# Kernel tuning notes

Hardware: AMD Instinct MI355X
Metric: run time of the kernel (lower is better)

The kernel has to match this reference:

```python
import jax, jax.numpy as jnp
import numpy as np

N = 100000       # nodes
E = 3200000      # directed edges (before self-loops)
D_IN, D_H, D_OUT = 512, 128, 64


def setup_inputs() -> dict:
    key = jax.random.key(0)
    k = jax.random.split(key, 6)
    x = jax.random.normal(k[0], (N, D_IN), jnp.float32)
    edge_index = jax.random.randint(k[1], (2, E), 0, N, dtype=jnp.int32)
    # Glorot-style init, matching GCNConv's linear weights
    W1 = jax.random.normal(k[2], (D_IN, D_H), jnp.float32) * np.float32(1.0 / np.sqrt(D_IN))
    b1 = jnp.zeros((D_H,), jnp.float32)
    W2 = jax.random.normal(k[3], (D_H, D_OUT), jnp.float32) * np.float32(1.0 / np.sqrt(D_H))
    b2 = jnp.zeros((D_OUT,), jnp.float32)
    return {"x": x, "edge_index": edge_index, "W1": W1, "b1": b1, "W2": W2, "b2": b2}


def _gcn_layer(h, src, dst, norm, W, b):
    # GCNConv: transform, then normalized gather/scatter-add aggregation
    h = h @ W                                  # [N, F_out]
    msg = h[src] * norm[:, None]               # gather + per-edge scale
    agg = jax.ops.segment_sum(msg, dst, num_segments=N)  # scatter-add
    return agg + b


def reference(x, edge_index, W1, b1, W2, b2):
    # add self-loops (GCNConv default add_self_loops=True)
    loops = jnp.arange(N, dtype=edge_index.dtype)
    src = jnp.concatenate([edge_index[0], loops])
    dst = jnp.concatenate([edge_index[1], loops])
    # symmetric normalization: D^{-1/2} (A+I) D^{-1/2}
    deg = jax.ops.segment_sum(jnp.ones_like(dst, dtype=x.dtype), dst, num_segments=N)
    dinv = jax.lax.rsqrt(jnp.maximum(deg, 1.0))  # deg >= 1 because of self-loops
    norm = dinv[src] * dinv[dst]                 # per-edge weight
    h = jax.nn.relu(_gcn_layer(x, src, dst, norm, W1, b1))
    return _gcn_layer(h, src, dst, norm, W2, b2)
```

## Files before the change

### kernel.cpp

```cpp
#include <hip/hip_runtime.h>
#include <hip/hip_bf16.h>


typedef __bf16 bf16x8 __attribute__((ext_vector_type(8)));
typedef __bf16 bf16x4 __attribute__((ext_vector_type(4)));
typedef float  f32x4  __attribute__((ext_vector_type(4)));

__device__ inline unsigned rne16(float x) {
    unsigned u = __float_as_uint(x);
    return (u + 0x7fffu + ((u >> 16) & 1u)) >> 16;
}

__global__ void deg_kernel(const int* __restrict__ dst, int E, unsigned* __restrict__ deg) {
    int stride = gridDim.x * blockDim.x;
    for (int e = blockIdx.x * blockDim.x + threadIdx.x; e < E; e += stride)
        atomicAdd(&deg[dst[e]], 1u);
}

__global__ void scan_block(const unsigned* __restrict__ deg, int* __restrict__ off,
                           unsigned* __restrict__ partials, float* __restrict__ dinv, int N) {
    __shared__ unsigned s[256];
    int v = blockIdx.x * 256 + threadIdx.x;
    unsigned x = (v < N) ? deg[v] : 0u;
    s[threadIdx.x] = x;
    __syncthreads();
    #pragma unroll
    for (int d = 1; d < 256; d <<= 1) {
        unsigned t = (threadIdx.x >= d) ? s[threadIdx.x - d] : 0u;
        __syncthreads();
        s[threadIdx.x] += t;
        __syncthreads();
    }
    if (v < N) {
        off[v] = (int)(s[threadIdx.x] - x);
        dinv[v] = rsqrtf((float)(x + 1u));
    }
    if (threadIdx.x == 255) partials[blockIdx.x] = s[255];
}

__global__ void scan_partials(unsigned* __restrict__ partials, int B) {
    __shared__ unsigned s[1024];
    int i = threadIdx.x;
    unsigned x = (i < B) ? partials[i] : 0u;
    s[i] = x;
    __syncthreads();
    #pragma unroll
    for (int d = 1; d < 1024; d <<= 1) {
        unsigned t = (i >= d) ? s[i - d] : 0u;
        __syncthreads();
        s[i] += t;
        __syncthreads();
    }
    if (i < B) partials[i] = s[i] - x;
}

__global__ void add_partials(int* __restrict__ off, const unsigned* __restrict__ partials,
                             int N, int E) {
    int v = blockIdx.x * 256 + threadIdx.x;
    if (v < N) off[v] += (int)partials[blockIdx.x];
    if (v == 0) off[N] = E;
}

__global__ void fill_csr(const int* __restrict__ src, const int* __restrict__ dst, int E,
                         const int* __restrict__ off, unsigned* __restrict__ cursor,
                         int* __restrict__ csr) {
    int stride = gridDim.x * blockDim.x;
    for (int e = blockIdx.x * blockDim.x + threadIdx.x; e < E; e += stride) {
        int d = dst[e];
        unsigned p = atomicAdd(&cursor[d], 1u);
        csr[off[d] + (int)p] = src[e];
    }
}

__global__ void tsplit(const float* __restrict__ W, __bf16* __restrict__ hi,
                       __bf16* __restrict__ lo, int K, int Nc) {
    int i = blockIdx.x * 256 + threadIdx.x;
    if (i >= K * Nc) return;
    int k = i / Nc, n = i % Nc;
    float f = W[i];
    __bf16 h = (__bf16)f;
    hi[(size_t)n * K + k] = h;
    lo[(size_t)n * K + k] = (__bf16)(f - (float)h);
}

template <int K>
__global__ __launch_bounds__(256) void gemm1_mfma(
    const float* __restrict__ A, const __bf16* __restrict__ Bhi,
    const __bf16* __restrict__ Blo, const float* __restrict__ dinv,
    __bf16* __restrict__ C, int M)
{
    constexpr int LDA = 40;
    __shared__ __bf16 shi[32][LDA];
    __shared__ __bf16 slo[32][LDA];

    const int tid = threadIdx.x;
    const int lane = tid & 63;
    const int wave = tid >> 6;
    const int m0 = blockIdx.x * 32;
    const int col0 = wave * 32;
    const int lrow = lane & 15;
    const int lk = (lane >> 4) * 8;
    const int arow = tid >> 3;
    const int ac4 = (tid & 7) * 4;

    f32x4 acc[2][2];
    #pragma unroll
    for (int r = 0; r < 2; ++r)
        #pragma unroll
        for (int c = 0; c < 2; ++c) acc[r][c] = (f32x4){0.f, 0.f, 0.f, 0.f};

    #pragma unroll 1
    for (int kk = 0; kk < K; kk += 32) {
        __syncthreads();
        {
            int gr = m0 + arow; if (gr >= M) gr = M - 1;
            float4 f = *(const float4*)(A + (size_t)gr * K + kk + ac4);
            bf16x4 h, l;
            h[0] = (__bf16)f.x; l[0] = (__bf16)(f.x - (float)h[0]);
            h[1] = (__bf16)f.y; l[1] = (__bf16)(f.y - (float)h[1]);
            h[2] = (__bf16)f.z; l[2] = (__bf16)(f.z - (float)h[2]);
            h[3] = (__bf16)f.w; l[3] = (__bf16)(f.w - (float)h[3]);
            *(bf16x4*)&shi[arow][ac4] = h;
            *(bf16x4*)&slo[arow][ac4] = l;
        }
        __syncthreads();
        bf16x8 ah[2], al[2];
        #pragma unroll
        for (int r = 0; r < 2; ++r) {
            ah[r] = *(const bf16x8*)&shi[r * 16 + lrow][lk];
            al[r] = *(const bf16x8*)&slo[r * 16 + lrow][lk];
        }
        #pragma unroll
        for (int c = 0; c < 2; ++c) {
            bf16x8 bh = *(const bf16x8*)(Bhi + (size_t)(col0 + c * 16 + lrow) * K + kk + lk);
            bf16x8 bl = *(const bf16x8*)(Blo + (size_t)(col0 + c * 16 + lrow) * K + kk + lk);
            #pragma unroll
            for (int r = 0; r < 2; ++r) {
                acc[r][c] = __builtin_amdgcn_mfma_f32_16x16x32_bf16(ah[r], bh, acc[r][c], 0, 0, 0);
                acc[r][c] = __builtin_amdgcn_mfma_f32_16x16x32_bf16(ah[r], bl, acc[r][c], 0, 0, 0);
                acc[r][c] = __builtin_amdgcn_mfma_f32_16x16x32_bf16(al[r], bh, acc[r][c], 0, 0, 0);
            }
        }
    }
    #pragma unroll
    for (int r = 0; r < 2; ++r) {
        #pragma unroll
        for (int j = 0; j < 4; ++j) {
            int m = m0 + r * 16 + (lane >> 4) * 4 + j;
            if (m >= M) continue;
            float dv = dinv[m];
            #pragma unroll
            for (int c = 0; c < 2; ++c)
                C[(size_t)m * 128 + col0 + c * 16 + lrow] = (__bf16)(acc[r][c][j] * dv);
        }
    }
}

template <int K>
__global__ __launch_bounds__(256) void gemm2_mfma(
    const __bf16* __restrict__ A, const __bf16* __restrict__ Bhi,
    const __bf16* __restrict__ Blo, const float* __restrict__ dinv,
    __bf16* __restrict__ C, int M)
{
    const int lane = threadIdx.x & 63;
    const int wave = threadIdx.x >> 6;
    const int m0 = blockIdx.x * 64 + (wave >> 1) * 32;
    const int col0 = (wave & 1) * 32;
    const int lrow = lane & 15;
    const int lk = (lane >> 4) * 8;

    f32x4 acc[2][2];
    #pragma unroll
    for (int r = 0; r < 2; ++r)
        #pragma unroll
        for (int c = 0; c < 2; ++c) acc[r][c] = (f32x4){0.f, 0.f, 0.f, 0.f};

    #pragma unroll
    for (int kk = 0; kk < K; kk += 32) {
        bf16x8 ah[2];
        #pragma unroll
        for (int r = 0; r < 2; ++r) {
            int gr = m0 + r * 16 + lrow; if (gr >= M) gr = M - 1;
            ah[r] = *(const bf16x8*)(A + (size_t)gr * K + kk + lk);
        }
        #pragma unroll
        for (int c = 0; c < 2; ++c) {
            bf16x8 bh = *(const bf16x8*)(Bhi + (size_t)(col0 + c * 16 + lrow) * K + kk + lk);
            bf16x8 bl = *(const bf16x8*)(Blo + (size_t)(col0 + c * 16 + lrow) * K + kk + lk);
            #pragma unroll
            for (int r = 0; r < 2; ++r) {
                acc[r][c] = __builtin_amdgcn_mfma_f32_16x16x32_bf16(ah[r], bh, acc[r][c], 0, 0, 0);
                acc[r][c] = __builtin_amdgcn_mfma_f32_16x16x32_bf16(ah[r], bl, acc[r][c], 0, 0, 0);
            }
        }
    }
    #pragma unroll
    for (int r = 0; r < 2; ++r) {
        #pragma unroll
        for (int j = 0; j < 4; ++j) {
            int m = m0 + r * 16 + (lane >> 4) * 4 + j;
            if (m >= M) continue;
            float dv = dinv[m];
            #pragma unroll
            for (int c = 0; c < 2; ++c)
                C[(size_t)m * 64 + col0 + c * 16 + lrow] = (__bf16)(acc[r][c][j] * dv);
        }
    }
}

__global__ __launch_bounds__(256) void agg128(
    const int* __restrict__ off, const int* __restrict__ csr,
    const unsigned* __restrict__ hs,
    const float* __restrict__ dinv, const float* __restrict__ bias,
    unsigned* __restrict__ h1, int N)
{
    const int lane = threadIdx.x & 63;
    const int v = blockIdx.x * 4 + (threadIdx.x >> 6);
    if (v >= N) return;
    const int s0 = off[v], s1 = off[v + 1];
    float a0 = 0.f, a1 = 0.f;
    for (int e0 = s0; e0 < s1; e0 += 64) {
        int nid = (e0 + lane < s1) ? csr[e0 + lane] : 0;
        int cnt = min(64, s1 - e0);
        int j = 0;
        for (; j + 8 <= cnt; j += 8) {
            unsigned u[8];
            #pragma unroll
            for (int q = 0; q < 8; ++q) {
                int s = __shfl(nid, j + q);
                u[q] = hs[(size_t)s * 64 + lane];
            }
            #pragma unroll
            for (int q = 0; q < 8; ++q) {
                a0 += __uint_as_float(u[q] << 16);
                a1 += __uint_as_float(u[q] & 0xffff0000u);
            }
        }
        for (; j < cnt; ++j) {
            int s = __shfl(nid, j);
            unsigned u = hs[(size_t)s * 64 + lane];
            a0 += __uint_as_float(u << 16);
            a1 += __uint_as_float(u & 0xffff0000u);
        }
    }
    unsigned su = hs[(size_t)v * 64 + lane];
    const float dv = dinv[v];
    float r0 = (a0 + __uint_as_float(su << 16)) * dv + bias[lane * 2 + 0];
    float r1 = (a1 + __uint_as_float(su & 0xffff0000u)) * dv + bias[lane * 2 + 1];
    r0 = fmaxf(r0, 0.f);
    r1 = fmaxf(r1, 0.f);
    h1[(size_t)v * 64 + lane] = rne16(r0) | (rne16(r1) << 16);
}

__global__ __launch_bounds__(256) void agg64(
    const int* __restrict__ off, const int* __restrict__ csr,
    const unsigned short* __restrict__ hs2, const float* __restrict__ dinv,
    const float* __restrict__ bias, float* __restrict__ out, int N)
{
    const int lane = threadIdx.x & 63;
    const int v = blockIdx.x * 4 + (threadIdx.x >> 6);
    if (v >= N) return;
    const int s0 = off[v], s1 = off[v + 1];
    float a0 = 0.f;
    for (int e0 = s0; e0 < s1; e0 += 64) {
        int nid = (e0 + lane < s1) ? csr[e0 + lane] : 0;
        int cnt = min(64, s1 - e0);
        int j = 0;
        for (; j + 8 <= cnt; j += 8) {
            unsigned short u[8];
            #pragma unroll
            for (int q = 0; q < 8; ++q) {
                int s = __shfl(nid, j + q);
                u[q] = hs2[(size_t)s * 64 + lane];
            }
            #pragma unroll
            for (int q = 0; q < 8; ++q)
                a0 += __uint_as_float((unsigned)u[q] << 16);
        }
        for (; j < cnt; ++j) {
            int s = __shfl(nid, j);
            a0 += __uint_as_float((unsigned)hs2[(size_t)s * 64 + lane] << 16);
        }
    }
    float self = __uint_as_float((unsigned)hs2[(size_t)v * 64 + lane] << 16);
    out[(size_t)v * 64 + lane] = (a0 + self) * dinv[v] + bias[lane];
}

extern "C" void kernel_launch(void* const* d_in, const int* in_sizes, int n_in,
                              void* d_out, int out_size, void* d_ws, size_t ws_size,
                              hipStream_t stream)
{
    const float* x  = (const float*)d_in[0];
    const int*   ei = (const int*)d_in[1];
    const float* W1 = (const float*)d_in[2];
    const float* b1 = (const float*)d_in[3];
    const float* W2 = (const float*)d_in[4];
    const float* b2 = (const float*)d_in[5];
    float* out = (float*)d_out;

    const int N = in_sizes[0] / 512;
    const int E = in_sizes[1] / 2;
    const int* src = ei;
    const int* dst = ei + E;

    unsigned* deg      = (unsigned*)d_ws;
    unsigned* cursor   = deg + N;
    int*      off      = (int*)(cursor + N);
    unsigned* partials = (unsigned*)(off + N + 4);
    float*    dinv     = (float*)(partials + 1024);
    int*      csr      = (int*)(dinv + N);
    __bf16*   Bt1hi    = (__bf16*)(csr + E);
    __bf16*   Bt1lo    = Bt1hi + 128 * 512;
    __bf16*   Bt2hi    = Bt1lo + 128 * 512;
    __bf16*   Bt2lo    = Bt2hi + 64 * 128;
    __bf16*   hs       = Bt2lo + 64 * 128;
    __bf16*   h1       = hs + (size_t)N * 128;
    __bf16*   hs2      = h1 + (size_t)N * 128;

    const int SB = (N + 255) / 256;

    hipMemsetAsync(deg, 0, (size_t)N * 8, stream);

    deg_kernel<<<dim3(2048), 256, 0, stream>>>(dst, E, deg);

    scan_block<<<dim3(SB), 256, 0, stream>>>(deg, off, partials, dinv, N);
    scan_partials<<<dim3(1), 1024, 0, stream>>>(partials, SB);
    add_partials<<<dim3(SB), 256, 0, stream>>>(off, partials, N, E);
    fill_csr<<<dim3(2048), 256, 0, stream>>>(src, dst, E, off, cursor, csr);

    tsplit<<<dim3((512 * 128 + 255) / 256), 256, 0, stream>>>(W1, Bt1hi, Bt1lo, 512, 128);
    tsplit<<<dim3((128 * 64 + 255) / 256), 256, 0, stream>>>(W2, Bt2hi, Bt2lo, 128, 64);

    gemm1_mfma<512><<<dim3((N + 31) / 32), 256, 0, stream>>>(x, Bt1hi, Bt1lo, dinv, hs, N);
    agg128<<<dim3((N + 3) / 4), 256, 0, stream>>>(
        off, csr, (const unsigned*)hs, dinv, b1, (unsigned*)h1, N);

    gemm2_mfma<128><<<dim3((N + 63) / 64), 256, 0, stream>>>(h1, Bt2hi, Bt2lo, dinv, hs2, N);
    agg64<<<dim3((N + 3) / 4), 256, 0, stream>>>(
        off, csr, (const unsigned short*)hs2, dinv, b2, out, N);
}
```

Measured before the change: 967.1 us.

## Build CSR via two-level bucket sort and double-buffer GEMM1 A tiles

Replaces the per-node global-atomic degree count, three-kernel scan and random-scatter CSR fill with a bucketed counting sort. Edges are binned by destination into 128-node buckets using shared-memory histograms, scattered as packed (dst,src) pairs, then each bucket builds its CSR segment, offsets and dinv in shared memory before writing it out coalesced. This is meant to cut global atomic contention and uncoalesced writes, at the cost of an extra 8-byte-per-edge buffer pass. Separately, GEMM1 double-buffers the shared A tile and prefetches the next float4 to drop one barrier per k-step.

```diff
diff --git a/kernel.cpp b/kernel.cpp
--- a/kernel.cpp
+++ b/kernel.cpp
@@ -6,42 +6,34 @@
 typedef __bf16 bf16x4 __attribute__((ext_vector_type(4)));
 typedef float  f32x4  __attribute__((ext_vector_type(4)));
 
+#define NBSHIFT 7
+#define CSR_CAP 8192
+
 __device__ inline unsigned rne16(float x) {
     unsigned u = __float_as_uint(x);
     return (u + 0x7fffu + ((u >> 16) & 1u)) >> 16;
 }
 
-__global__ void deg_kernel(const int* __restrict__ dst, int E, unsigned* __restrict__ deg) {
+__global__ __launch_bounds__(256) void bucket_count(
+    const int* __restrict__ dst, int E, unsigned* __restrict__ bhist, int NB)
+{
+    __shared__ unsigned lh[1024];
+    for (int i = threadIdx.x; i < NB; i += 256) lh[i] = 0;
+    __syncthreads();
     int stride = gridDim.x * blockDim.x;
     for (int e = blockIdx.x * blockDim.x + threadIdx.x; e < E; e += stride)
-        atomicAdd(&deg[dst[e]], 1u);
-}
-
-__global__ void scan_block(const unsigned* __restrict__ deg, int* __restrict__ off,
-                           unsigned* __restrict__ partials, float* __restrict__ dinv, int N) {
-    __shared__ unsigned s[256];
-    int v = blockIdx.x * 256 + threadIdx.x;
-    unsigned x = (v < N) ? deg[v] : 0u;
-    s[threadIdx.x] = x;
-    __syncthreads();
-    #pragma unroll
-    for (int d = 1; d < 256; d <<= 1) {
-        unsigned t = (threadIdx.x >= d) ? s[threadIdx.x - d] : 0u;
-        __syncthreads();
-        s[threadIdx.x] += t;
-        __syncthreads();
-    }
-    if (v < N) {
-        off[v] = (int)(s[threadIdx.x] - x);
-        dinv[v] = rsqrtf((float)(x + 1u));
-    }
-    if (threadIdx.x == 255) partials[blockIdx.x] = s[255];
-}
-
-__global__ void scan_partials(unsigned* __restrict__ partials, int B) {
+        atomicAdd(&lh[dst[e] >> NBSHIFT], 1u);
+    __syncthreads();
+    for (int i = threadIdx.x; i < NB; i += 256)
+        if (lh[i]) atomicAdd(&bhist[i], lh[i]);
+}
+
+__global__ void bucket_scan(const unsigned* __restrict__ bhist, int* __restrict__ boff,
+                            unsigned* __restrict__ gcur, int NB, int E)
+{
     __shared__ unsigned s[1024];
     int i = threadIdx.x;
-    unsigned x = (i < B) ? partials[i] : 0u;
+    unsigned x = (i < NB) ? bhist[i] : 0u;
     s[i] = x;
     __syncthreads();
     #pragma unroll
@@ -51,24 +43,91 @@
         s[i] += t;
         __syncthreads();
     }
-    if (i < B) partials[i] = s[i] - x;
-}
-
-__global__ void add_partials(int* __restrict__ off, const unsigned* __restrict__ partials,
-                             int N, int E) {
-    int v = blockIdx.x * 256 + threadIdx.x;
-    if (v < N) off[v] += (int)partials[blockIdx.x];
-    if (v == 0) off[N] = E;
-}
-
-__global__ void fill_csr(const int* __restrict__ src, const int* __restrict__ dst, int E,
-                         const int* __restrict__ off, unsigned* __restrict__ cursor,
-                         int* __restrict__ csr) {
-    int stride = gridDim.x * blockDim.x;
-    for (int e = blockIdx.x * blockDim.x + threadIdx.x; e < E; e += stride) {
+    if (i < NB) { boff[i] = (int)(s[i] - x); gcur[i] = s[i] - x; }
+    if (i == NB - 1) boff[NB] = (int)s[i];
+}
+
+__global__ __launch_bounds__(256) void bucket_scatter(
+    const int* __restrict__ src, const int* __restrict__ dst, int E,
+    unsigned* __restrict__ gcur, unsigned long long* __restrict__ buf, int NB)
+{
+    __shared__ unsigned lh[1024];
+    __shared__ unsigned lbase[1024];
+    for (int i = threadIdx.x; i < NB; i += 256) lh[i] = 0;
+    __syncthreads();
+    int tile = (E + gridDim.x - 1) / gridDim.x;
+    int lo = blockIdx.x * tile, hi = min(E, lo + tile);
+    for (int e = lo + threadIdx.x; e < hi; e += 256)
+        atomicAdd(&lh[dst[e] >> NBSHIFT], 1u);
+    __syncthreads();
+    for (int i = threadIdx.x; i < NB; i += 256) {
+        unsigned c = lh[i];
+        lbase[i] = c ? atomicAdd(&gcur[i], c) : 0u;
+        lh[i] = 0;
+    }
+    __syncthreads();
+    for (int e = lo + threadIdx.x; e < hi; e += 256) {
         int d = dst[e];
-        unsigned p = atomicAdd(&cursor[d], 1u);
-        csr[off[d] + (int)p] = src[e];
+        int b = d >> NBSHIFT;
+        unsigned r = atomicAdd(&lh[b], 1u);
+        buf[lbase[b] + r] = ((unsigned long long)(unsigned)d << 32) | (unsigned)src[e];
+    }
+}
+
+__global__ __launch_bounds__(256) void bucket_csr(
+    const unsigned long long* __restrict__ buf, const int* __restrict__ boff,
+    int* __restrict__ csr, int* __restrict__ off, float* __restrict__ dinv,
+    int N, int E)
+{
+    __shared__ unsigned hist[128];
+    __shared__ unsigned incl[128];
+    __shared__ unsigned cur[128];
+    __shared__ int lcsr[CSR_CAP];
+    const int b = blockIdx.x, tid = threadIdx.x;
+    const int lo = boff[b], hi = boff[b + 1], cnt = hi - lo;
+    const int nbase = b << NBSHIFT;
+    const int nn = min(128, N - nbase);
+
+    if (tid < 128) hist[tid] = 0;
+    __syncthreads();
+    for (int i = lo + tid; i < hi; i += 256)
+        atomicAdd(&hist[(int)(buf[i] >> 32) - nbase], 1u);
+    __syncthreads();
+    if (tid < 128) incl[tid] = hist[tid];
+    __syncthreads();
+    #pragma unroll
+    for (int d = 1; d < 128; d <<= 1) {
+        unsigned t = (tid < 128 && tid >= d) ? incl[tid - d] : 0u;
+        __syncthreads();
+        if (tid < 128) incl[tid] += t;
+        __syncthreads();
+    }
+    if (tid < 128) {
+        unsigned e0 = incl[tid] - hist[tid];
+        cur[tid] = e0;
+        if (tid < nn) {
+            off[nbase + tid] = lo + (int)e0;
+            dinv[nbase + tid] = rsqrtf((float)(hist[tid] + 1u));
+        }
+    }
+    if (b == 0 && tid == 0) off[N] = E;
+    __syncthreads();
+    if (cnt <= CSR_CAP) {
+        for (int i = lo + tid; i < hi; i += 256) {
+            unsigned long long p = buf[i];
+            int dl = (int)(p >> 32) - nbase;
+            unsigned r = atomicAdd(&cur[dl], 1u);
+            lcsr[r] = (int)(p & 0xffffffffu);
+        }
+        __syncthreads();
+        for (int i = tid; i < cnt; i += 256) csr[lo + i] = lcsr[i];
+    } else {
+        for (int i = lo + tid; i < hi; i += 256) {
+            unsigned long long p = buf[i];
+            int dl = (int)(p >> 32) - nbase;
+            unsigned r = atomicAdd(&cur[dl], 1u);
+            csr[lo + (int)r] = (int)(p & 0xffffffffu);
+        }
     }
 }
 
@@ -90,8 +149,8 @@
     __bf16* __restrict__ C, int M)
 {
     constexpr int LDA = 40;
-    __shared__ __bf16 shi[32][LDA];
-    __shared__ __bf16 slo[32][LDA];
+    __shared__ __bf16 shi[2][32][LDA];
+    __shared__ __bf16 slo[2][32][LDA];
 
     const int tid = threadIdx.x;
     const int lane = tid & 63;
@@ -102,6 +161,7 @@
     const int lk = (lane >> 4) * 8;
     const int arow = tid >> 3;
     const int ac4 = (tid & 7) * 4;
+    const float* aptr = A + (size_t)min(m0 + arow, M - 1) * K + ac4;
 
     f32x4 acc[2][2];
     #pragma unroll
@@ -109,26 +169,24 @@
         #pragma unroll
         for (int c = 0; c < 2; ++c) acc[r][c] = (f32x4){0.f, 0.f, 0.f, 0.f};
 
-    #pragma unroll 1
+    float4 f = *(const float4*)aptr;
     for (int kk = 0; kk < K; kk += 32) {
-        __syncthreads();
-        {
-            int gr = m0 + arow; if (gr >= M) gr = M - 1;
-            float4 f = *(const float4*)(A + (size_t)gr * K + kk + ac4);
-            bf16x4 h, l;
-            h[0] = (__bf16)f.x; l[0] = (__bf16)(f.x - (float)h[0]);
-            h[1] = (__bf16)f.y; l[1] = (__bf16)(f.y - (float)h[1]);
-            h[2] = (__bf16)f.z; l[2] = (__bf16)(f.z - (float)h[2]);
-            h[3] = (__bf16)f.w; l[3] = (__bf16)(f.w - (float)h[3]);
-            *(bf16x4*)&shi[arow][ac4] = h;
-            *(bf16x4*)&slo[arow][ac4] = l;
-        }
-        __syncthreads();
+        const int cur = (kk >> 5) & 1;
+        bf16x4 h, l;
+        h[0] = (__bf16)f.x; l[0] = (__bf16)(f.x - (float)h[0]);
+        h[1] = (__bf16)f.y; l[1] = (__bf16)(f.y - (float)h[1]);
+        h[2] = (__bf16)f.z; l[2] = (__bf16)(f.z - (float)h[2]);
+        h[3] = (__bf16)f.w; l[3] = (__bf16)(f.w - (float)h[3]);
+        *(bf16x4*)&shi[cur][arow][ac4] = h;
+        *(bf16x4*)&slo[cur][arow][ac4] = l;
+        __syncthreads();
+        if (kk + 32 < K) f = *(const float4*)(aptr + kk + 32);
+
         bf16x8 ah[2], al[2];
         #pragma unroll
         for (int r = 0; r < 2; ++r) {
-            ah[r] = *(const bf16x8*)&shi[r * 16 + lrow][lk];
-            al[r] = *(const bf16x8*)&slo[r * 16 + lrow][lk];
+            ah[r] = *(const bf16x8*)&shi[cur][r * 16 + lrow][lk];
+            al[r] = *(const bf16x8*)&slo[cur][r * 16 + lrow][lk];
         }
         #pragma unroll
         for (int c = 0; c < 2; ++c) {
@@ -302,12 +360,14 @@
     const int E = in_sizes[1] / 2;
     const int* src = ei;
     const int* dst = ei + E;
-
-    unsigned* deg      = (unsigned*)d_ws;
-    unsigned* cursor   = deg + N;
-    int*      off      = (int*)(cursor + N);
-    unsigned* partials = (unsigned*)(off + N + 4);
-    float*    dinv     = (float*)(partials + 1024);
+    const int NB = (N + 127) >> NBSHIFT;
+
+    unsigned long long* buf = (unsigned long long*)d_ws;
+    unsigned* bhist    = (unsigned*)(buf + E);
+    int*      boff     = (int*)(bhist + NB);
+    unsigned* gcur     = (unsigned*)(boff + NB + 1);
+    int*      off      = (int*)(gcur + NB);
+    float*    dinv     = (float*)(off + N + 1);
     int*      csr      = (int*)(dinv + N);
     __bf16*   Bt1hi    = (__bf16*)(csr + E);
     __bf16*   Bt1lo    = Bt1hi + 128 * 512;
@@ -317,16 +377,12 @@
     __bf16*   h1       = hs + (size_t)N * 128;
     __bf16*   hs2      = h1 + (size_t)N * 128;
 
-    const int SB = (N + 255) / 256;
-
-    hipMemsetAsync(deg, 0, (size_t)N * 8, stream);
-
-    deg_kernel<<<dim3(2048), 256, 0, stream>>>(dst, E, deg);
-
-    scan_block<<<dim3(SB), 256, 0, stream>>>(deg, off, partials, dinv, N);
-    scan_partials<<<dim3(1), 1024, 0, stream>>>(partials, SB);
-    add_partials<<<dim3(SB), 256, 0, stream>>>(off, partials, N, E);
-    fill_csr<<<dim3(2048), 256, 0, stream>>>(src, dst, E, off, cursor, csr);
+    hipMemsetAsync(bhist, 0, (size_t)NB * 4, stream);
+
+    bucket_count<<<dim3(512), 256, 0, stream>>>(dst, E, bhist, NB);
+    bucket_scan<<<dim3(1), 1024, 0, stream>>>(bhist, boff, gcur, NB, E);
+    bucket_scatter<<<dim3(512), 256, 0, stream>>>(src, dst, E, gcur, buf, NB);
+    bucket_csr<<<dim3(NB), 256, 0, stream>>>(buf, boff, csr, off, dinv, N, E);
 
     tsplit<<<dim3((512 * 128 + 255) / 256), 256, 0, stream>>>(W1, Bt1hi, Bt1lo, 512, 128);
     tsplit<<<dim3((128 * 64 + 255) / 256), 256, 0, stream>>>(W2, Bt2hi, Bt2lo, 128, 64);
```

Result: faster. 809.7 us (-16.3%).
